# Optimization experiments

Measured on AMD Instinct MI355X. Metric: run time of the kernel, lower is better.

Reference implementation:

```python
import jax, jax.numpy as jnp
import numpy as np

B, N, DEG = 32, 1024, 8
E = B * N * DEG
NT = B * N
F_IN, HID, EDIM, NR, HD = 64, 128, 16, 16, 4
NEG = 0.2  # leaky_relu negative slope (alpha)
K1 = int(np.ceil(0.8 * N))    # 820 kept nodes per graph after pool1
K2 = int(np.ceil(0.8 * K1))   # 656 kept nodes per graph after pool2


def setup_inputs() -> dict:
    key = jax.random.key(0)
    ks = jax.random.split(key, 20)
    nrm = lambda i, shp, s=0.05: jax.random.normal(ks[i], shp, jnp.float32) * s
    x = jax.random.normal(ks[0], (NT, F_IN), jnp.float32)
    off = (jnp.arange(B) * N)[:, None]
    src = (jax.random.randint(ks[1], (B, N * DEG), 0, N) + off).reshape(-1)
    dst = (jax.random.randint(ks[2], (B, N * DEG), 0, N) + off).reshape(-1)
    edge_index = jnp.stack([src, dst]).astype(jnp.int32)
    edge_attr = jax.random.normal(ks[3], (E, EDIM), jnp.float32)
    action = jax.random.normal(ks[4], (B, NR), jnp.float32)
    return dict(
        x=x, edge_attr=edge_attr, action=action,
        W1l=nrm(5, (F_IN, HD * HID)), b1l=jnp.zeros(HD * HID),
        W1r=nrm(6, (F_IN, HD * HID)), b1r=jnp.zeros(HD * HID),
        W1e=nrm(7, (EDIM, HD * HID)), att1=nrm(8, (HD, HID)), bias1=jnp.zeros(HID),
        W2l=nrm(9, (HID, HD * HID)), b2l=jnp.zeros(HD * HID),
        W2r=nrm(10, (HID, HD * HID)), b2r=jnp.zeros(HD * HID),
        W2e=nrm(11, (EDIM, HD * HID)), att2=nrm(12, (HD, HID)), bias2=jnp.zeros(HID),
        p1=nrm(13, (HID,), 0.1), p2=nrm(14, (HID,), 0.1),
        Wf1=nrm(15, (2 * HID + NR, HID)), bf1=jnp.zeros(HID),
        Wf2=nrm(16, (HID, HID)), bf2=jnp.zeros(HID),
        Wf3=nrm(17, (HID, 1), 0.003), bf3=jnp.zeros(1),
        edge_index=edge_index,
    )


def _gatv2(x, edge_index, edge_attr, edge_mask, Wl, bl, Wr, br, We, att, bias):
    # PyG GATv2Conv, concat=False (mean over heads), eval mode (no dropout).
    src, dst = edge_index[0], edge_index[1]
    n = x.shape[0]
    xl = (x @ Wl + bl).reshape(n, HD, HID)   # source transform (x_j)
    xr = (x @ Wr + br).reshape(n, HD, HID)   # target transform (x_i)
    ef = (edge_attr @ We).reshape(-1, HD, HID)
    m = jax.nn.leaky_relu(xl[src] + xr[dst] + ef, NEG)          # [E,H,C]
    logits = jnp.where(edge_mask[:, None], (m * att).sum(-1), -1e9)  # [E,H]
    mx = jax.ops.segment_max(logits, dst, num_segments=n)
    a = jnp.exp(logits - mx[dst])
    den = jax.ops.segment_sum(a, dst, num_segments=n)
    alpha = (a / (den[dst] + 1e-16)) * edge_mask[:, None]       # softmax per dst, masked edges zeroed
    out = jax.ops.segment_sum(xl[src] * alpha[..., None], dst, num_segments=n)
    return out.mean(axis=1) + bias


def _topk(x, node_mask, p, k):
    # PyG TopKPooling: score = x@p/||p||, gate = tanh(score), keep top-k per graph.
    score = (x @ p) / (jnp.linalg.norm(p) + 1e-16)
    gate = jnp.tanh(score)
    s = jnp.where(node_mask, score, -jnp.inf).reshape(B, N)
    idx = jax.lax.top_k(s, k)[1]                                # [B,k]
    keep = jnp.zeros((B, N), bool).at[jnp.arange(B)[:, None], idx].set(True).reshape(-1)
    return x * gate[:, None], keep


def reference(x, edge_attr, action, W1l, b1l, W1r, b1r, W1e, att1, bias1,
              W2l, b2l, W2r, b2r, W2e, att2, bias2, p1, p2,
              Wf1, bf1, Wf2, bf2, Wf3, bf3, edge_index):
    src, dst = edge_index[0], edge_index[1]
    em0 = jnp.ones((E,), bool)
    h = jax.nn.relu(_gatv2(x, edge_index, edge_attr, em0,
                           W1l, b1l, W1r, b1r, W1e, att1, bias1))
    h, keep1 = _topk(h, jnp.ones((NT,), bool), p1, K1)
    em1 = keep1[src] & keep1[dst]
    h = jax.nn.relu(_gatv2(h, edge_index, edge_attr, em1,
                           W2l, b2l, W2r, b2r, W2e, att2, bias2))
    h, keep2 = _topk(h, keep1, p2, K2)
    hb = h.reshape(B, N, HID)
    mb = keep2.reshape(B, N)[..., None]
    gmx = jnp.where(mb, hb, -jnp.inf).max(axis=1)               # global max pool over kept nodes
    gav = (hb * mb).sum(axis=1) / K2                            # global mean pool (K2 kept per graph)
    z = jnp.concatenate([gmx, gav, action], axis=1)             # [B, 2*HID+NR]
    z = jax.nn.relu(z @ Wf1 + bf1)
    z = jax.nn.relu(z @ Wf2 + bf2)
    return z @ Wf3 + bf3
```

## Files before the change

kernel.cpp:

```cpp
#include <hip/hip_runtime.h>
#include <math.h>

#define NTN 32768
#define NBG 32
#define NN  1024
#define EE  262144
#define FIN 64
#define HIDC 128
#define HD  4
#define HC  512
#define EDIM 16
#define NR  16
#define KP1 820
#define KP2 656
#define NEGS 0.2f
#define NPB 2

template<int K>
__global__ __launch_bounds__(256) void gemm_node2(const float* __restrict__ A,
                                                  const float* __restrict__ Wl,
                                                  const float* __restrict__ bl,
                                                  const float* __restrict__ Wr,
                                                  const float* __restrict__ br,
                                                  const float* __restrict__ gs,
                                                  float* __restrict__ Cl,
                                                  float* __restrict__ Cr) {
    __shared__ float a_s[K][16];
    __shared__ float g_s[16];
    int t = threadIdx.x;
    int row0 = blockIdx.x * 16;
    if (t < 16) g_s[t] = gs ? tanhf(gs[row0 + t]) : 1.0f;
    __syncthreads();
    for (int i = t; i < 16 * K; i += 256) {
        int r = i / K, k = i % K;
        a_s[k][r] = A[(size_t)(row0 + r) * K + k] * g_s[r];
    }
    __syncthreads();
    int c0 = t, c1 = t + 256;
    float accl0[16], accl1[16], accr0[16], accr1[16];
    float bl0 = bl[c0], bl1 = bl[c1], br0 = br[c0], br1 = br[c1];
    #pragma unroll
    for (int r = 0; r < 16; r++) { accl0[r] = bl0; accl1[r] = bl1; accr0[r] = br0; accr1[r] = br1; }
    for (int k = 0; k < K; k++) {
        float wl0 = Wl[(size_t)k * HC + c0], wl1 = Wl[(size_t)k * HC + c1];
        float wr0 = Wr[(size_t)k * HC + c0], wr1 = Wr[(size_t)k * HC + c1];
        const float4* ap = (const float4*)&a_s[k][0];
        float4 A0 = ap[0], A1 = ap[1], A2 = ap[2], A3 = ap[3];
        float av[16] = {A0.x, A0.y, A0.z, A0.w, A1.x, A1.y, A1.z, A1.w,
                        A2.x, A2.y, A2.z, A2.w, A3.x, A3.y, A3.z, A3.w};
        #pragma unroll
        for (int r = 0; r < 16; r++) {
            accl0[r] += av[r] * wl0; accl1[r] += av[r] * wl1;
            accr0[r] += av[r] * wr0; accr1[r] += av[r] * wr1;
        }
    }
    for (int r = 0; r < 16; r++) {
        Cl[(size_t)(row0 + r) * HC + c0] = accl0[r];
        Cl[(size_t)(row0 + r) * HC + c1] = accl1[r];
        Cr[(size_t)(row0 + r) * HC + c0] = accr0[r];
        Cr[(size_t)(row0 + r) * HC + c1] = accr1[r];
    }
}

__global__ void edge_hist(const int* __restrict__ dst, const int* __restrict__ src,
                          const int* __restrict__ keep, int* __restrict__ deg) {
    int e = blockIdx.x * 256 + threadIdx.x;
    if (e < EE) {
        if (keep && (!keep[src[e]] || !keep[dst[e]])) return;
        atomicAdd(&deg[dst[e]], 1);
    }
}

__global__ __launch_bounds__(1024) void scan_deg(const int* __restrict__ deg,
                                                 int* __restrict__ off, int* __restrict__ cur) {
    __shared__ int s[1024];
    int t = threadIdx.x;
    int base = t * 32;
    int local[32];
    int sum = 0;
    #pragma unroll
    for (int i = 0; i < 32; i++) { local[i] = deg[base + i]; sum += local[i]; }
    s[t] = sum;
    for (int o = 1; o < 1024; o <<= 1) {
        __syncthreads();
        int v = (t >= o) ? s[t - o] : 0;
        __syncthreads();
        s[t] += v;
    }
    __syncthreads();
    int run = s[t] - sum;
    #pragma unroll
    for (int i = 0; i < 32; i++) { off[base + i] = run; cur[base + i] = run; run += local[i]; }
    if (t == 1023) off[NTN] = s[1023];
}

__global__ void edge_scatter(const int* __restrict__ dst, const int* __restrict__ src,
                             const int* __restrict__ keep, const float* __restrict__ ea,
                             int* __restrict__ cur,
                             int* __restrict__ esrc, float* __restrict__ eaP) {
    int e = blockIdx.x * 256 + threadIdx.x;
    if (e < EE) {
        if (keep && (!keep[src[e]] || !keep[dst[e]])) return;
        int p = atomicAdd(&cur[dst[e]], 1);
        esrc[p] = src[e];
        const float4* s4 = (const float4*)(ea + (size_t)e * EDIM);
        float4* d4 = (float4*)(eaP + (size_t)p * EDIM);
        d4[0] = s4[0]; d4[1] = s4[1]; d4[2] = s4[2]; d4[3] = s4[3];
    }
}

__global__ __launch_bounds__(64) void prep_pn(const float* __restrict__ p1,
                                              const float* __restrict__ p2,
                                              float* __restrict__ pn) {
    int t = threadIdx.x;
    float a = p1[t] * p1[t] + p1[t + 64] * p1[t + 64];
    float b = p2[t] * p2[t] + p2[t + 64] * p2[t + 64];
    #pragma unroll
    for (int sft = 32; sft; sft >>= 1) { a += __shfl_xor(a, sft, 64); b += __shfl_xor(b, sft, 64); }
    if (t == 0) { pn[0] = 1.f / (sqrtf(a) + 1e-16f); pn[1] = 1.f / (sqrtf(b) + 1e-16f); }
}

__global__ __launch_bounds__(256) void gat_dst(
        const float* __restrict__ xl, const float* __restrict__ xr,
        const float* __restrict__ eaP, const float* __restrict__ We,
        const float* __restrict__ att, const float* __restrict__ bias,
        const float* __restrict__ pvec, const float* __restrict__ pnInv,
        const int* __restrict__ esrc, const int* __restrict__ off,
        float* __restrict__ out, float* __restrict__ score) {
    int t = threadIdx.x;
    int w = t >> 6, lane = t & 63;
    int c = w * HIDC + lane * 2;
    __shared__ float red[NPB][HC];
    __shared__ float red2[NPB][HIDC];
    float we0[EDIM], we1[EDIM];
    #pragma unroll
    for (int k = 0; k < EDIM; k++) {
        we0[k] = We[(size_t)k * HC + c];
        we1[k] = We[(size_t)k * HC + c + 1];
    }
    float at0 = att[c], at1 = att[c + 1];
    int d0 = blockIdx.x * NPB;

    for (int n = 0; n < NPB; n++) {
        int d = d0 + n;
        float2 xrv = *(const float2*)&xr[((unsigned)d << 9) + c];
        int e0 = off[d], e1 = off[d + 1];
        float m = -3e38f, den = 0.f, acc0 = 0.f, acc1 = 0.f;
        int ei = e0;
        for (; ei + 2 <= e1; ei += 2) {
            int sA = esrc[ei], sB = esrc[ei + 1];
            const float4* eA = (const float4*)(eaP + ((size_t)ei << 4));
            float4 A0 = eA[0], A1 = eA[1], A2 = eA[2], A3 = eA[3];
            float4 B0 = eA[4], B1 = eA[5], B2 = eA[6], B3 = eA[7];
            float2 xlA = *(const float2*)&xl[((unsigned)sA << 9) + c];
            float2 xlB = *(const float2*)&xl[((unsigned)sB << 9) + c];
            float avA[16] = {A0.x, A0.y, A0.z, A0.w, A1.x, A1.y, A1.z, A1.w,
                             A2.x, A2.y, A2.z, A2.w, A3.x, A3.y, A3.z, A3.w};
            float avB[16] = {B0.x, B0.y, B0.z, B0.w, B1.x, B1.y, B1.z, B1.w,
                             B2.x, B2.y, B2.z, B2.w, B3.x, B3.y, B3.z, B3.w};
            float efA0 = 0.f, efA1 = 0.f, efB0 = 0.f, efB1 = 0.f;
            #pragma unroll
            for (int k = 0; k < EDIM; k++) {
                efA0 += avA[k] * we0[k]; efA1 += avA[k] * we1[k];
                efB0 += avB[k] * we0[k]; efB1 += avB[k] * we1[k];
            }
            float vA0 = xlA.x + xrv.x + efA0; vA0 = vA0 > 0.f ? vA0 : NEGS * vA0;
            float vA1 = xlA.y + xrv.y + efA1; vA1 = vA1 > 0.f ? vA1 : NEGS * vA1;
            float vB0 = xlB.x + xrv.x + efB0; vB0 = vB0 > 0.f ? vB0 : NEGS * vB0;
            float vB1 = xlB.y + xrv.y + efB1; vB1 = vB1 > 0.f ? vB1 : NEGS * vB1;
            float pA = vA0 * at0 + vA1 * at1;
            float pB = vB0 * at0 + vB1 * at1;
            #pragma unroll
            for (int sft = 32; sft; sft >>= 1) {
                pA += __shfl_xor(pA, sft, 64);
                pB += __shfl_xor(pB, sft, 64);
            }
            if (pA > m + 8.f) {
                float sc = __expf(m - pA);
                den = den * sc + 1.f; acc0 = acc0 * sc + xlA.x; acc1 = acc1 * sc + xlA.y;
                m = pA;
            } else {
                float wt = __expf(pA - m);
                den += wt; acc0 += wt * xlA.x; acc1 += wt * xlA.y;
            }
            if (pB > m + 8.f) {
                float sc = __expf(m - pB);
                den = den * sc + 1.f; acc0 = acc0 * sc + xlB.x; acc1 = acc1 * sc + xlB.y;
                m = pB;
            } else {
                float wt = __expf(pB - m);
                den += wt; acc0 += wt * xlB.x; acc1 += wt * xlB.y;
            }
        }
        if (ei < e1) {
            int s = esrc[ei];
            const float4* eA = (const float4*)(eaP + ((size_t)ei << 4));
            float4 A0 = eA[0], A1 = eA[1], A2 = eA[2], A3 = eA[3];
            float2 xlA = *(const float2*)&xl[((unsigned)s << 9) + c];
            float avA[16] = {A0.x, A0.y, A0.z, A0.w, A1.x, A1.y, A1.z, A1.w,
                             A2.x, A2.y, A2.z, A2.w, A3.x, A3.y, A3.z, A3.w};
            float ef0 = 0.f, ef1 = 0.f;
            #pragma unroll
            for (int k = 0; k < EDIM; k++) { ef0 += avA[k] * we0[k]; ef1 += avA[k] * we1[k]; }
            float v0 = xlA.x + xrv.x + ef0; v0 = v0 > 0.f ? v0 : NEGS * v0;
            float v1 = xlA.y + xrv.y + ef1; v1 = v1 > 0.f ? v1 : NEGS * v1;
            float p = v0 * at0 + v1 * at1;
            #pragma unroll
            for (int sft = 32; sft; sft >>= 1) p += __shfl_xor(p, sft, 64);
            if (p > m + 8.f) {
                float sc = __expf(m - p);
                den = den * sc + 1.f; acc0 = acc0 * sc + xlA.x; acc1 = acc1 * sc + xlA.y;
                m = p;
            } else {
                float wt = __expf(p - m);
                den += wt; acc0 += wt * xlA.x; acc1 += wt * xlA.y;
            }
        }
        float inv = 1.f / (den + 1e-16f);
        red[n][c] = acc0 * inv;
        red[n][c + 1] = acc1 * inv;
    }
    __syncthreads();
    {
        int n2 = t >> 7, tc = t & 127;
        float v = (red[n2][tc] + red[n2][tc + 128] + red[n2][tc + 256] + red[n2][tc + 384]) * 0.25f
                  + bias[tc];
        v = fmaxf(v, 0.f);
        out[((unsigned)(d0 + n2) << 7) + tc] = v;
        red2[n2][tc] = v * pvec[tc];
    }
    __syncthreads();
    if (t < 128) {
        int n3 = t >> 6, l2 = t & 63;
        float sv = red2[n3][l2] + red2[n3][l2 + 64];
        #pragma unroll
        for (int sft = 32; sft; sft >>= 1) sv += __shfl_xor(sv, sft, 64);
        if (l2 == 0) score[d0 + n3] = sv * pnInv[0];
    }
}

__global__ __launch_bounds__(512) void topk_sel(const float* __restrict__ score,
                                                const int* __restrict__ mask, int k,
                                                int* __restrict__ keep) {
    __shared__ float v[NN];
    __shared__ short id[NN];
    int g = blockIdx.x, t = threadIdx.x;
    for (int i = t; i < NN; i += 512) {
        int n = g * NN + i;
        bool mk = mask ? (mask[n] != 0) : true;
        v[i] = mk ? score[n] : -INFINITY;
        id[i] = (short)i;
    }
    __syncthreads();
    for (int kk = 2; kk <= NN; kk <<= 1) {
        for (int j = kk >> 1; j > 0; j >>= 1) {
            #pragma unroll 2
            for (int i = t; i < NN; i += 512) {
                int ixj = i ^ j;
                if (ixj > i) {
                    bool up = ((i & kk) == 0);
                    float a = v[i], b2 = v[ixj];
                    short ia = id[i], ib = id[ixj];
                    bool aFirst = (a > b2) || (a == b2 && ia < ib);
                    if (up ? !aFirst : aFirst) { v[i] = b2; v[ixj] = a; id[i] = ib; id[ixj] = ia; }
                }
            }
            __syncthreads();
        }
    }
    for (int i = t; i < NN; i += 512) keep[g * NN + id[i]] = (i < k) ? 1 : 0;
}

__global__ __launch_bounds__(512) void gpool(const float* __restrict__ h,
                                             const int* __restrict__ keep,
                                             const float* __restrict__ score,
                                             const float* __restrict__ action,
                                             float* __restrict__ z) {
    int g = blockIdx.x, t = threadIdx.x;
    int c = t & 127, ch = t >> 7;
    __shared__ float gt_s[NN];
    __shared__ char kp_s[NN];
    __shared__ float smx[4][HIDC], ssm[4][HIDC];
    for (int i = t; i < NN; i += 512) {
        int n = g * NN + i;
        int kk = keep[n];
        kp_s[i] = (char)kk;
        gt_s[i] = kk ? tanhf(score[n]) : 0.f;
    }
    __syncthreads();
    float mx = -INFINITY, sm = 0.f;
    for (int n = ch * 256; n < ch * 256 + 256; n++) {
        if (kp_s[n]) {
            float v = h[(size_t)(g * NN + n) * HIDC + c] * gt_s[n];
            mx = fmaxf(mx, v);
            sm += v;
        }
    }
    smx[ch][c] = mx; ssm[ch][c] = sm;
    __syncthreads();
    if (t < HIDC) {
        mx = fmaxf(fmaxf(smx[0][t], smx[1][t]), fmaxf(smx[2][t], smx[3][t]));
        sm = ssm[0][t] + ssm[1][t] + ssm[2][t] + ssm[3][t];
        z[g * 272 + t] = mx;
        z[g * 272 + 128 + t] = sm / (float)KP2;
        if (t < NR) z[g * 272 + 256 + t] = action[g * NR + t];
    }
}

__global__ __launch_bounds__(128) void mlp(const float* __restrict__ z,
                                           const float* __restrict__ Wf1, const float* __restrict__ bf1,
                                           const float* __restrict__ Wf2, const float* __restrict__ bf2,
                                           const float* __restrict__ Wf3, const float* __restrict__ bf3,
                                           float* __restrict__ out) {
    int g = blockIdx.x, t = threadIdx.x;
    __shared__ float zs[272], z1[HIDC], z2[HIDC], r[HIDC];
    for (int i = t; i < 272; i += 128) zs[i] = z[g * 272 + i];
    __syncthreads();
    float a = bf1[t];
    for (int k = 0; k < 272; k++) a += zs[k] * Wf1[(size_t)k * HIDC + t];
    z1[t] = fmaxf(a, 0.f);
    __syncthreads();
    a = bf2[t];
    for (int k = 0; k < HIDC; k++) a += z1[k] * Wf2[(size_t)k * HIDC + t];
    z2[t] = fmaxf(a, 0.f);
    __syncthreads();
    r[t] = z2[t] * Wf3[t];
    __syncthreads();
    for (int s = 64; s; s >>= 1) { if (t < s) r[t] += r[t + s]; __syncthreads(); }
    if (t == 0) out[g] = r[0] + bf3[0];
}

extern "C" void kernel_launch(void* const* d_in, const int* in_sizes, int n_in,
                              void* d_out, int out_size, void* d_ws, size_t ws_size,
                              hipStream_t stream) {
    const float* x    = (const float*)d_in[0];
    const float* ea   = (const float*)d_in[1];
    const float* act  = (const float*)d_in[2];
    const float* W1l  = (const float*)d_in[3];
    const float* b1l  = (const float*)d_in[4];
    const float* W1r  = (const float*)d_in[5];
    const float* b1r  = (const float*)d_in[6];
    const float* W1e  = (const float*)d_in[7];
    const float* att1 = (const float*)d_in[8];
    const float* bias1= (const float*)d_in[9];
    const float* W2l  = (const float*)d_in[10];
    const float* b2l  = (const float*)d_in[11];
    const float* W2r  = (const float*)d_in[12];
    const float* b2r  = (const float*)d_in[13];
    const float* W2e  = (const float*)d_in[14];
    const float* att2 = (const float*)d_in[15];
    const float* bias2= (const float*)d_in[16];
    const float* p1   = (const float*)d_in[17];
    const float* p2   = (const float*)d_in[18];
    const float* Wf1  = (const float*)d_in[19];
    const float* bf1  = (const float*)d_in[20];
    const float* Wf2  = (const float*)d_in[21];
    const float* bf2  = (const float*)d_in[22];
    const float* Wf3  = (const float*)d_in[23];
    const float* bf3  = (const float*)d_in[24];
    const int*   eix  = (const int*)d_in[25];
    const int* srcA = eix;
    const int* dstA = eix + EE;

    float* ws    = (float*)d_ws;
    float* xl    = ws;
    float* xr    = xl + (size_t)NTN * HC;
    float* h     = xr + (size_t)NTN * HC;
    float* score1= h + (size_t)NTN * HIDC;
    float* score2= score1 + NTN;
    float* zbuf  = score2 + NTN;
    float* pn    = zbuf + NBG * 272;
    int* keep1 = (int*)(pn + 2);
    int* keep2 = keep1 + NTN;
    int* deg   = keep2 + NTN;
    int* off   = deg + NTN;
    int* cur   = off + NTN + 1;
    int* deg2  = cur + NTN;
    int* off2  = deg2 + NTN;
    int* cur2  = off2 + NTN + 1;
    int* esrc  = cur2 + NTN;
    int* esrc2 = esrc + EE;
    float* eaP  = (float*)(esrc2 + EE);
    float* eaP2 = eaP + (size_t)EE * EDIM;

    hipMemsetAsync(deg, 0, NTN * sizeof(int), stream);
    prep_pn<<<1, 64, 0, stream>>>(p1, p2, pn);
    edge_hist<<<EE / 256, 256, 0, stream>>>(dstA, srcA, nullptr, deg);
    scan_deg<<<1, 1024, 0, stream>>>(deg, off, cur);
    edge_scatter<<<EE / 256, 256, 0, stream>>>(dstA, srcA, nullptr, ea, cur, esrc, eaP);

    gemm_node2<FIN><<<NTN / 16, 256, 0, stream>>>(x, W1l, b1l, W1r, b1r, nullptr, xl, xr);
    gat_dst<<<NTN / NPB, 256, 0, stream>>>(xl, xr, eaP, W1e, att1, bias1, p1, pn, esrc, off, h, score1);

    topk_sel<<<NBG, 512, 0, stream>>>(score1, nullptr, KP1, keep1);

    hipMemsetAsync(deg2, 0, NTN * sizeof(int), stream);
    edge_hist<<<EE / 256, 256, 0, stream>>>(dstA, srcA, keep1, deg2);
    scan_deg<<<1, 1024, 0, stream>>>(deg2, off2, cur2);
    edge_scatter<<<EE / 256, 256, 0, stream>>>(dstA, srcA, keep1, ea, cur2, esrc2, eaP2);

    gemm_node2<HIDC><<<NTN / 16, 256, 0, stream>>>(h, W2l, b2l, W2r, b2r, score1, xl, xr);
    gat_dst<<<NTN / NPB, 256, 0, stream>>>(xl, xr, eaP2, W2e, att2, bias2, p2, pn + 1, esrc2, off2, h, score2);

    topk_sel<<<NBG, 512, 0, stream>>>(score2, keep1, KP2, keep2);

    gpool<<<NBG, 512, 0, stream>>>(h, keep2, score2, act, zbuf);
    mlp<<<NBG, 128, 0, stream>>>(zbuf, Wf1, bf1, Wf2, bf2, Wf3, bf3, (float*)d_out);
}
```

Measured before the change: 635.4 us.

## Restrict layer-2 GEMM to kept nodes, widen GAT unroll, fuse tail kernels

The layer-2 node GEMM now processes only the top-k kept nodes, using a compact list written by topk_sel, instead of all nodes. The GAT kernel handles 4 destinations per block with a block-index swizzle and processes 4 edges per iteration to raise memory-level parallelism. The second top-k, global pooling and MLP are fused into one tail kernel, and prep_pn is folded into scan_deg, which removes several launches. Rows of xl/xr for dropped nodes are left stale, which is safe only because masked edges never read them.

After: 678.9 us. +6.8%, slower.

```diff
diff --git a/kernel.cpp b/kernel.cpp
--- a/kernel.cpp
+++ b/kernel.cpp
@@ -13,8 +13,9 @@
 #define NR  16
 #define KP1 820
 #define KP2 656
+#define NKEPT (KP1 * NBG)
 #define NEGS 0.2f
-#define NPB 2
+#define NPB 4
 
 template<int K>
 __global__ __launch_bounds__(256) void gemm_node2(const float* __restrict__ A,
@@ -23,17 +24,23 @@
                                                   const float* __restrict__ Wr,
                                                   const float* __restrict__ br,
                                                   const float* __restrict__ gs,
+                                                  const int* __restrict__ ids,
                                                   float* __restrict__ Cl,
                                                   float* __restrict__ Cr) {
     __shared__ float a_s[K][16];
     __shared__ float g_s[16];
+    __shared__ int rid_s[16];
     int t = threadIdx.x;
     int row0 = blockIdx.x * 16;
-    if (t < 16) g_s[t] = gs ? tanhf(gs[row0 + t]) : 1.0f;
+    if (t < 16) {
+        int rid = ids ? ids[row0 + t] : (row0 + t);
+        rid_s[t] = rid;
+        g_s[t] = gs ? tanhf(gs[rid]) : 1.0f;
+    }
     __syncthreads();
     for (int i = t; i < 16 * K; i += 256) {
         int r = i / K, k = i % K;
-        a_s[k][r] = A[(size_t)(row0 + r) * K + k] * g_s[r];
+        a_s[k][r] = A[(size_t)rid_s[r] * K + k] * g_s[r];
     }
     __syncthreads();
     int c0 = t, c1 = t + 256;
@@ -55,10 +62,11 @@
         }
     }
     for (int r = 0; r < 16; r++) {
-        Cl[(size_t)(row0 + r) * HC + c0] = accl0[r];
-        Cl[(size_t)(row0 + r) * HC + c1] = accl1[r];
-        Cr[(size_t)(row0 + r) * HC + c0] = accr0[r];
-        Cr[(size_t)(row0 + r) * HC + c1] = accr1[r];
+        size_t base = (size_t)rid_s[r] * HC;
+        Cl[base + c0] = accl0[r];
+        Cl[base + c1] = accl1[r];
+        Cr[base + c0] = accr0[r];
+        Cr[base + c1] = accr1[r];
     }
 }
 
@@ -72,7 +80,10 @@
 }
 
 __global__ __launch_bounds__(1024) void scan_deg(const int* __restrict__ deg,
-                                                 int* __restrict__ off, int* __restrict__ cur) {
+                                                 int* __restrict__ off, int* __restrict__ cur,
+                                                 const float* __restrict__ p1,
+                                                 const float* __restrict__ p2,
+                                                 float* __restrict__ pn) {
     __shared__ int s[1024];
     int t = threadIdx.x;
     int base = t * 32;
@@ -92,6 +103,13 @@
     #pragma unroll
     for (int i = 0; i < 32; i++) { off[base + i] = run; cur[base + i] = run; run += local[i]; }
     if (t == 1023) off[NTN] = s[1023];
+    if (pn && t < 64) {
+        float a = p1[t] * p1[t] + p1[t + 64] * p1[t + 64];
+        float b = p2[t] * p2[t] + p2[t + 64] * p2[t + 64];
+        #pragma unroll
+        for (int sft = 32; sft; sft >>= 1) { a += __shfl_xor(a, sft, 64); b += __shfl_xor(b, sft, 64); }
+        if (t == 0) { pn[0] = 1.f / (sqrtf(a) + 1e-16f); pn[1] = 1.f / (sqrtf(b) + 1e-16f); }
+    }
 }
 
 __global__ void edge_scatter(const int* __restrict__ dst, const int* __restrict__ src,
@@ -109,24 +127,16 @@
     }
 }
 
-__global__ __launch_bounds__(64) void prep_pn(const float* __restrict__ p1,
-                                              const float* __restrict__ p2,
-                                              float* __restrict__ pn) {
-    int t = threadIdx.x;
-    float a = p1[t] * p1[t] + p1[t + 64] * p1[t + 64];
-    float b = p2[t] * p2[t] + p2[t + 64] * p2[t + 64];
-    #pragma unroll
-    for (int sft = 32; sft; sft >>= 1) { a += __shfl_xor(a, sft, 64); b += __shfl_xor(b, sft, 64); }
-    if (t == 0) { pn[0] = 1.f / (sqrtf(a) + 1e-16f); pn[1] = 1.f / (sqrtf(b) + 1e-16f); }
-}
-
 __global__ __launch_bounds__(256) void gat_dst(
         const float* __restrict__ xl, const float* __restrict__ xr,
         const float* __restrict__ eaP, const float* __restrict__ We,
         const float* __restrict__ att, const float* __restrict__ bias,
         const float* __restrict__ pvec, const float* __restrict__ pnInv,
         const int* __restrict__ esrc, const int* __restrict__ off,
-        float* __restrict__ out, float* __restrict__ score) {
+        float* __restrict__ out, float* __restrict__ score, int nblk) {
+    int bid = blockIdx.x;
+    int swz = (bid & 7) * (nblk >> 3) + (bid >> 3);
+    int d0 = swz * NPB;
     int t = threadIdx.x;
     int w = t >> 6, lane = t & 63;
     int c = w * HIDC + lane * 2;
@@ -139,81 +149,71 @@
         we1[k] = We[(size_t)k * HC + c + 1];
     }
     float at0 = att[c], at1 = att[c + 1];
-    int d0 = blockIdx.x * NPB;
 
     for (int n = 0; n < NPB; n++) {
         int d = d0 + n;
-        float2 xrv = *(const float2*)&xr[((unsigned)d << 9) + c];
+        float2 xrv = *(const float2*)&xr[((size_t)d << 9) + c];
         int e0 = off[d], e1 = off[d + 1];
         float m = -3e38f, den = 0.f, acc0 = 0.f, acc1 = 0.f;
         int ei = e0;
-        for (; ei + 2 <= e1; ei += 2) {
-            int sA = esrc[ei], sB = esrc[ei + 1];
-            const float4* eA = (const float4*)(eaP + ((size_t)ei << 4));
-            float4 A0 = eA[0], A1 = eA[1], A2 = eA[2], A3 = eA[3];
-            float4 B0 = eA[4], B1 = eA[5], B2 = eA[6], B3 = eA[7];
-            float2 xlA = *(const float2*)&xl[((unsigned)sA << 9) + c];
-            float2 xlB = *(const float2*)&xl[((unsigned)sB << 9) + c];
-            float avA[16] = {A0.x, A0.y, A0.z, A0.w, A1.x, A1.y, A1.z, A1.w,
-                             A2.x, A2.y, A2.z, A2.w, A3.x, A3.y, A3.z, A3.w};
-            float avB[16] = {B0.x, B0.y, B0.z, B0.w, B1.x, B1.y, B1.z, B1.w,
-                             B2.x, B2.y, B2.z, B2.w, B3.x, B3.y, B3.z, B3.w};
-            float efA0 = 0.f, efA1 = 0.f, efB0 = 0.f, efB1 = 0.f;
-            #pragma unroll
-            for (int k = 0; k < EDIM; k++) {
-                efA0 += avA[k] * we0[k]; efA1 += avA[k] * we1[k];
-                efB0 += avB[k] * we0[k]; efB1 += avB[k] * we1[k];
-            }
-            float vA0 = xlA.x + xrv.x + efA0; vA0 = vA0 > 0.f ? vA0 : NEGS * vA0;
-            float vA1 = xlA.y + xrv.y + efA1; vA1 = vA1 > 0.f ? vA1 : NEGS * vA1;
-            float vB0 = xlB.x + xrv.x + efB0; vB0 = vB0 > 0.f ? vB0 : NEGS * vB0;
-            float vB1 = xlB.y + xrv.y + efB1; vB1 = vB1 > 0.f ? vB1 : NEGS * vB1;
-            float pA = vA0 * at0 + vA1 * at1;
-            float pB = vB0 * at0 + vB1 * at1;
+        for (; ei + 4 <= e1; ei += 4) {
+            int s[4]; float2 xv[4]; float p[4];
+            #pragma unroll
+            for (int j = 0; j < 4; j++) s[j] = esrc[ei + j];
+            #pragma unroll
+            for (int j = 0; j < 4; j++) xv[j] = *(const float2*)&xl[((size_t)s[j] << 9) + c];
+            #pragma unroll
+            for (int j = 0; j < 4; j++) {
+                const float4* eap = (const float4*)(eaP + ((size_t)(ei + j) << 4));
+                float4 E0 = eap[0], E1 = eap[1], E2 = eap[2], E3 = eap[3];
+                float ev[16] = {E0.x, E0.y, E0.z, E0.w, E1.x, E1.y, E1.z, E1.w,
+                                E2.x, E2.y, E2.z, E2.w, E3.x, E3.y, E3.z, E3.w};
+                float ef0 = 0.f, ef1 = 0.f;
+                #pragma unroll
+                for (int k = 0; k < EDIM; k++) { ef0 += ev[k] * we0[k]; ef1 += ev[k] * we1[k]; }
+                float v0 = xv[j].x + xrv.x + ef0; v0 = v0 > 0.f ? v0 : NEGS * v0;
+                float v1 = xv[j].y + xrv.y + ef1; v1 = v1 > 0.f ? v1 : NEGS * v1;
+                p[j] = v0 * at0 + v1 * at1;
+            }
             #pragma unroll
             for (int sft = 32; sft; sft >>= 1) {
-                pA += __shfl_xor(pA, sft, 64);
-                pB += __shfl_xor(pB, sft, 64);
-            }
-            if (pA > m + 8.f) {
-                float sc = __expf(m - pA);
-                den = den * sc + 1.f; acc0 = acc0 * sc + xlA.x; acc1 = acc1 * sc + xlA.y;
-                m = pA;
-            } else {
-                float wt = __expf(pA - m);
-                den += wt; acc0 += wt * xlA.x; acc1 += wt * xlA.y;
-            }
-            if (pB > m + 8.f) {
-                float sc = __expf(m - pB);
-                den = den * sc + 1.f; acc0 = acc0 * sc + xlB.x; acc1 = acc1 * sc + xlB.y;
-                m = pB;
-            } else {
-                float wt = __expf(pB - m);
-                den += wt; acc0 += wt * xlB.x; acc1 += wt * xlB.y;
-            }
-        }
-        if (ei < e1) {
+                #pragma unroll
+                for (int j = 0; j < 4; j++) p[j] += __shfl_xor(p[j], sft, 64);
+            }
+            #pragma unroll
+            for (int j = 0; j < 4; j++) {
+                if (p[j] > m + 8.f) {
+                    float sc = __expf(m - p[j]);
+                    den = den * sc + 1.f; acc0 = acc0 * sc + xv[j].x; acc1 = acc1 * sc + xv[j].y;
+                    m = p[j];
+                } else {
+                    float wt = __expf(p[j] - m);
+                    den += wt; acc0 += wt * xv[j].x; acc1 += wt * xv[j].y;
+                }
+            }
+        }
+        for (; ei < e1; ei++) {
             int s = esrc[ei];
-            const float4* eA = (const float4*)(eaP + ((size_t)ei << 4));
-            float4 A0 = eA[0], A1 = eA[1], A2 = eA[2], A3 = eA[3];
-            float2 xlA = *(const float2*)&xl[((unsigned)s << 9) + c];
-            float avA[16] = {A0.x, A0.y, A0.z, A0.w, A1.x, A1.y, A1.z, A1.w,
-                             A2.x, A2.y, A2.z, A2.w, A3.x, A3.y, A3.z, A3.w};
+            const float4* eap = (const float4*)(eaP + ((size_t)ei << 4));
+            float4 E0 = eap[0], E1 = eap[1], E2 = eap[2], E3 = eap[3];
+            float2 xv = *(const float2*)&xl[((size_t)s << 9) + c];
+            float ev[16] = {E0.x, E0.y, E0.z, E0.w, E1.x, E1.y, E1.z, E1.w,
+                            E2.x, E2.y, E2.z, E2.w, E3.x, E3.y, E3.z, E3.w};
             float ef0 = 0.f, ef1 = 0.f;
             #pragma unroll
-            for (int k = 0; k < EDIM; k++) { ef0 += avA[k] * we0[k]; ef1 += avA[k] * we1[k]; }
-            float v0 = xlA.x + xrv.x + ef0; v0 = v0 > 0.f ? v0 : NEGS * v0;
-            float v1 = xlA.y + xrv.y + ef1; v1 = v1 > 0.f ? v1 : NEGS * v1;
+            for (int k = 0; k < EDIM; k++) { ef0 += ev[k] * we0[k]; ef1 += ev[k] * we1[k]; }
+            float v0 = xv.x + xrv.x + ef0; v0 = v0 > 0.f ? v0 : NEGS * v0;
+            float v1 = xv.y + xrv.y + ef1; v1 = v1 > 0.f ? v1 : NEGS * v1;
             float p = v0 * at0 + v1 * at1;
             #pragma unroll
             for (int sft = 32; sft; sft >>= 1) p += __shfl_xor(p, sft, 64);
             if (p > m + 8.f) {
                 float sc = __expf(m - p);
-                den = den * sc + 1.f; acc0 = acc0 * sc + xlA.x; acc1 = acc1 * sc + xlA.y;
+                den = den * sc + 1.f; acc0 = acc0 * sc + xv.x; acc1 = acc1 * sc + xv.y;
                 m = p;
             } else {
                 float wt = __expf(p - m);
-                den += wt; acc0 += wt * xlA.x; acc1 += wt * xlA.y;
+                den += wt; acc0 += wt * xv.x; acc1 += wt * xv.y;
             }
         }
         float inv = 1.f / (den + 1e-16f);
@@ -221,16 +221,17 @@
         red[n][c + 1] = acc1 * inv;
     }
     __syncthreads();
-    {
-        int n2 = t >> 7, tc = t & 127;
+    #pragma unroll
+    for (int pass = 0; pass < NPB / 2; pass++) {
+        int n2 = pass * 2 + (t >> 7), tc = t & 127;
         float v = (red[n2][tc] + red[n2][tc + 128] + red[n2][tc + 256] + red[n2][tc + 384]) * 0.25f
                   + bias[tc];
         v = fmaxf(v, 0.f);
-        out[((unsigned)(d0 + n2) << 7) + tc] = v;
+        out[((size_t)(d0 + n2) << 7) + tc] = v;
         red2[n2][tc] = v * pvec[tc];
     }
     __syncthreads();
-    if (t < 128) {
+    {
         int n3 = t >> 6, l2 = t & 63;
         float sv = red2[n3][l2] + red2[n3][l2 + 64];
         #pragma unroll
@@ -241,7 +242,7 @@
 
 __global__ __launch_bounds__(512) void topk_sel(const float* __restrict__ score,
                                                 const int* __restrict__ mask, int k,
-                                                int* __restrict__ keep) {
+                                                int* __restrict__ keep, int* __restrict__ klist) {
     __shared__ float v[NN];
     __shared__ short id[NN];
     int g = blockIdx.x, t = threadIdx.x;
@@ -268,32 +269,68 @@
             __syncthreads();
         }
     }
-    for (int i = t; i < NN; i += 512) keep[g * NN + id[i]] = (i < k) ? 1 : 0;
-}
-
-__global__ __launch_bounds__(512) void gpool(const float* __restrict__ h,
-                                             const int* __restrict__ keep,
-                                             const float* __restrict__ score,
-                                             const float* __restrict__ action,
-                                             float* __restrict__ z) {
+    for (int i = t; i < NN; i += 512) {
+        int kp = (i < k) ? 1 : 0;
+        keep[g * NN + id[i]] = kp;
+        if (klist && kp) klist[g * k + i] = g * NN + id[i];
+    }
+}
+
+__global__ __launch_bounds__(512) void tail(const float* __restrict__ score,
+                                            const int* __restrict__ mask,
+                                            const float* __restrict__ h,
+                                            const float* __restrict__ action,
+                                            const float* __restrict__ Wf1, const float* __restrict__ bf1,
+                                            const float* __restrict__ Wf2, const float* __restrict__ bf2,
+                                            const float* __restrict__ Wf3, const float* __restrict__ bf3,
+                                            float* __restrict__ out) {
     int g = blockIdx.x, t = threadIdx.x;
-    int c = t & 127, ch = t >> 7;
+    __shared__ float v[NN];
+    __shared__ short id[NN];
     __shared__ float gt_s[NN];
     __shared__ char kp_s[NN];
     __shared__ float smx[4][HIDC], ssm[4][HIDC];
+    __shared__ float zs[2 * HIDC + NR], z1[HIDC], z2[HIDC], rr[HIDC];
     for (int i = t; i < NN; i += 512) {
         int n = g * NN + i;
-        int kk = keep[n];
-        kp_s[i] = (char)kk;
-        gt_s[i] = kk ? tanhf(score[n]) : 0.f;
-    }
-    __syncthreads();
+        bool mk = (mask[n] != 0);
+        v[i] = mk ? score[n] : -INFINITY;
+        id[i] = (short)i;
+        kp_s[i] = 0;
+        gt_s[i] = 0.f;
+    }
+    __syncthreads();
+    for (int kk = 2; kk <= NN; kk <<= 1) {
+        for (int j = kk >> 1; j > 0; j >>= 1) {
+            #pragma unroll 2
+            for (int i = t; i < NN; i += 512) {
+                int ixj = i ^ j;
+                if (ixj > i) {
+                    bool up = ((i & kk) == 0);
+                    float a = v[i], b2 = v[ixj];
+                    short ia = id[i], ib = id[ixj];
+                    bool aFirst = (a > b2) || (a == b2 && ia < ib);
+                    if (up ? !aFirst : aFirst) { v[i] = b2; v[ixj] = a; id[i] = ib; id[ixj] = ia; }
+                }
+            }
+            __syncthreads();
+        }
+    }
+    for (int i = t; i < NN; i += 512) {
+        if (i < KP2) {
+            int nid = id[i];
+            kp_s[nid] = 1;
+            gt_s[nid] = tanhf(score[g * NN + nid]);
+        }
+    }
+    __syncthreads();
+    int c = t & 127, ch = t >> 7;
     float mx = -INFINITY, sm = 0.f;
     for (int n = ch * 256; n < ch * 256 + 256; n++) {
         if (kp_s[n]) {
-            float v = h[(size_t)(g * NN + n) * HIDC + c] * gt_s[n];
-            mx = fmaxf(mx, v);
-            sm += v;
+            float hv = h[(size_t)(g * NN + n) * HIDC + c] * gt_s[n];
+            mx = fmaxf(mx, hv);
+            sm += hv;
         }
     }
     smx[ch][c] = mx; ssm[ch][c] = sm;
@@ -301,33 +338,29 @@
     if (t < HIDC) {
         mx = fmaxf(fmaxf(smx[0][t], smx[1][t]), fmaxf(smx[2][t], smx[3][t]));
         sm = ssm[0][t] + ssm[1][t] + ssm[2][t] + ssm[3][t];
-        z[g * 272 + t] = mx;
-        z[g * 272 + 128 + t] = sm / (float)KP2;
-        if (t < NR) z[g * 272 + 256 + t] = action[g * NR + t];
-    }
-}
-
-__global__ __launch_bounds__(128) void mlp(const float* __restrict__ z,
-                                           const float* __restrict__ Wf1, const float* __restrict__ bf1,
-                                           const float* __restrict__ Wf2, const float* __restrict__ bf2,
-                                           const float* __restrict__ Wf3, const float* __restrict__ bf3,
-                                           float* __restrict__ out) {
-    int g = blockIdx.x, t = threadIdx.x;
-    __shared__ float zs[272], z1[HIDC], z2[HIDC], r[HIDC];
-    for (int i = t; i < 272; i += 128) zs[i] = z[g * 272 + i];
-    __syncthreads();
-    float a = bf1[t];
-    for (int k = 0; k < 272; k++) a += zs[k] * Wf1[(size_t)k * HIDC + t];
-    z1[t] = fmaxf(a, 0.f);
-    __syncthreads();
-    a = bf2[t];
-    for (int k = 0; k < HIDC; k++) a += z1[k] * Wf2[(size_t)k * HIDC + t];
-    z2[t] = fmaxf(a, 0.f);
-    __syncthreads();
-    r[t] = z2[t] * Wf3[t];
-    __syncthreads();
-    for (int s = 64; s; s >>= 1) { if (t < s) r[t] += r[t + s]; __syncthreads(); }
-    if (t == 0) out[g] = r[0] + bf3[0];
+        zs[t] = mx;
+        zs[HIDC + t] = sm / (float)KP2;
+        if (t < NR) zs[2 * HIDC + t] = action[g * NR + t];
+    }
+    __syncthreads();
+    if (t < HIDC) {
+        float a = bf1[t];
+        for (int k = 0; k < 2 * HIDC + NR; k++) a += zs[k] * Wf1[(size_t)k * HIDC + t];
+        z1[t] = fmaxf(a, 0.f);
+    }
+    __syncthreads();
+    if (t < HIDC) {
+        float a = bf2[t];
+        for (int k = 0; k < HIDC; k++) a += z1[k] * Wf2[(size_t)k * HIDC + t];
+        z2[t] = fmaxf(a, 0.f);
+        rr[t] = z2[t] * Wf3[t];
+    }
+    __syncthreads();
+    for (int s = 64; s; s >>= 1) {
+        if (t < s) rr[t] += rr[t + s];
+        __syncthreads();
+    }
+    if (t == 0) out[g] = rr[0] + bf3[0];
 }
 
 extern "C" void kernel_launch(void* const* d_in, const int* in_sizes, int n_in,
@@ -368,11 +401,10 @@
     float* h     = xr + (size_t)NTN * HC;
     float* score1= h + (size_t)NTN * HIDC;
     float* score2= score1 + NTN;
-    float* zbuf  = score2 + NTN;
-    float* pn    = zbuf + NBG * 272;
+    float* pn    = score2 + NTN;
     int* keep1 = (int*)(pn + 2);
-    int* keep2 = keep1 + NTN;
-    int* deg   = keep2 + NTN;
+    int* klist = keep1 + NTN;
+    int* deg   = klist + NKEPT;
     int* off   = deg + NTN;
     int* cur   = off + NTN + 1;
     int* deg2  = cur + NTN;
@@ -384,26 +416,23 @@
     float* eaP2 = eaP + (size_t)EE * EDIM;
 
     hipMemsetAsync(deg, 0, NTN * sizeof(int), stream);
-    prep_pn<<<1, 64, 0, stream>>>(p1, p2, pn);
     edge_hist<<<EE / 256, 256, 0, stream>>>(dstA, srcA, nullptr, deg);
-    scan_deg<<<1, 1024, 0, stream>>>(deg, off, cur);
+    scan_deg<<<1, 1024, 0, stream>>>(deg, off, cur, p1, p2, pn);
     edge_scatter<<<EE / 256, 256, 0, stream>>>(dstA, srcA, nullptr, ea, cur, esrc, eaP);
 
-    gemm_node2<FIN><<<NTN / 16, 256, 0, stream>>>(x, W1l, b1l, W1r, b1r, nullptr, xl, xr);
-    gat_dst<<<NTN / NPB, 256, 0, stream>>>(xl, xr, eaP, W1e, att1, bias1, p1, pn, esrc, off, h, score1);
-
-    topk_sel<<<NBG, 512, 0, stream>>>(score1, nullptr, KP1, keep1);
+    gemm_node2<FIN><<<NTN / 16, 256, 0, stream>>>(x, W1l, b1l, W1r, b1r, nullptr, nullptr, xl, xr);
+    gat_dst<<<NTN / NPB, 256, 0, stream>>>(xl, xr, eaP, W1e, att1, bias1, p1, pn, esrc, off, h, score1, NTN / NPB);
+
+    topk_sel<<<NBG, 512, 0, stream>>>(score1, nullptr, KP1, keep1, klist);
 
     hipMemsetAsync(deg2, 0, NTN * sizeof(int), stream);
     edge_hist<<<EE / 256, 256, 0, stream>>>(dstA, srcA, keep1, deg2);
-    scan_deg<<<1, 1024, 0, stream>>>(deg2, off2, cur2);
+    scan_deg<<<1, 1024, 0, stream>>>(deg2, off2, cur2, nullptr, nullptr, nullptr);
     edge_scatter<<<EE / 256, 256, 0, stream>>>(dstA, srcA, keep1, ea, cur2, esrc2, eaP2);
 
-    gemm_node2<HIDC><<<NTN / 16, 256, 0, stream>>>(h, W2l, b2l, W2r, b2r, score1, xl, xr);
-    gat_dst<<<NTN / NPB, 256, 0, stream>>>(xl, xr, eaP2, W2e, att2, bias2, p2, pn + 1, esrc2, off2, h, score2);
-
-    topk_sel<<<NBG, 512, 0, stream>>>(score2, keep1, KP2, keep2);
-
-    gpool<<<NBG, 512, 0, stream>>>(h, keep2, score2, act, zbuf);
-    mlp<<<NBG, 128, 0, stream>>>(zbuf, Wf1, bf1, Wf2, bf2, Wf3, bf3, (float*)d_out);
-}
+    gemm_node2<HIDC><<<NKEPT / 16, 256, 0, stream>>>(h, W2l, b2l, W2r, b2r, score1, klist, xl, xr);
+    gat_dst<<<NTN / NPB, 256, 0, stream>>>(xl, xr, eaP2, W2e, att2, bias2, p2, pn + 1, esrc2, off2, h, score2, NTN / NPB);
+
+    tail<<<NBG, 512, 0, stream>>>(score2, keep1, h, act,
+                                  Wf1, bf1, Wf2, bf2, Wf3, bf3, (float*)d_out);
+}
```
